# Optimization experiments

Hardware: AMD Instinct MI355X
Metric: run time of the kernel (lower is better)

Reference implementation:

```python
import jax, jax.numpy as jnp
import numpy as np

B, L, D, H, R = 2, 128, 256, 8, 4
DK = D // H  # 32
EPS = 1e-6


def setup_inputs() -> dict:
    key = jax.random.key(0)
    ks = jax.random.split(key, 12)
    q = jax.random.normal(ks[0], (B, L, D), jnp.float32)
    k = jax.random.normal(ks[1], (B, L, D), jnp.float32)
    v = jax.random.normal(ks[2], (B, L, D), jnp.float32)
    t = jnp.sort(jax.random.uniform(ks[3], (B, L), jnp.float32), axis=-1)
    omega = jax.random.uniform(ks[4], (B, L, L), jnp.float32)
    mask = jnp.triu(jnp.ones((L, L), bool), 1)  # True = masked (causal)
    xav = (2.0 / (D + D)) ** 0.5
    Wq = jax.random.normal(ks[5], (D, H * DK), jnp.float32) * xav
    Wk = jax.random.normal(ks[6], (D, H * DK), jnp.float32) * xav
    Wv = jax.random.normal(ks[7], (D, H * DK), jnp.float32) * xav
    s = jax.random.uniform(ks[8], (R,), jnp.float32) + 0.1  # ODE time-decay scales
    fc_w = jax.random.normal(ks[9], (H * DK, D), jnp.float32) * xav
    fc_b = jnp.zeros((D,), jnp.float32)
    ln_g = jnp.ones((D,), jnp.float32)
    ln_b = jnp.zeros((D,), jnp.float32)
    return {"q": q, "k": k, "v": v, "t": t, "omega": omega, "mask": mask,
            "Wq": Wq, "Wk": Wk, "Wv": Wv, "s": s,
            "fc_w": fc_w, "fc_b": fc_b, "ln_g": ln_g, "ln_b": ln_b}


def _ode_proj(x, W, phi):
    # x: (B,L,D), W: (D,H*DK), phi: (B,L,L,R) time kernel
    p = x @ W                                       # (B,L,H*DK)
    y = p[:, None, :, None, :] * phi[..., None]     # (B,L,L,R,H*DK)
    y = y.reshape(B, L, L, R, H, DK)
    return y.transpose(0, 4, 1, 2, 3, 5)            # (B,H,L,L,R,DK)


def reference(q, k, v, t, omega, mask, Wq, Wk, Wv, s, fc_w, fc_b, ln_g, ln_b):
    temp = DK ** 0.5
    residual = q
    # pre-LayerNorm on q (normalize_before=True)
    mu = q.mean(-1, keepdims=True)
    var = q.var(-1, keepdims=True)
    qn = (q - mu) / jnp.sqrt(var + EPS) * ln_g + ln_b
    # continuous-time kernel phi[b,i,j,r] = exp(-|t_i - t_j| * s_r)
    dt = jnp.abs(t[:, :, None] - t[:, None, :])     # (B,L,L)
    phi = jnp.exp(-dt[..., None] * s)               # (B,L,L,R)
    q6 = _ode_proj(qn, Wq, phi)                     # (B,H,L,L,R,DK)
    k6 = _ode_proj(k, Wk, phi)
    v6 = _ode_proj(v, Wv, phi)
    # attn = (q/temp * k * omega).sum(-1).sum(-1)
    attn = jnp.einsum('bhijrd,bhijrd,bij->bhij', q6 / temp, k6, omega)
    attn = jnp.where(mask[None, None, :, :], -1e9, attn)
    attn = jax.nn.softmax(attn, axis=-1)            # (B,H,L,L)
    vsum = v6.sum(axis=4)                           # sum over R -> (B,H,L,L,DK)
    out = jnp.einsum('bhij,bhijd->bhid', attn, vsum)  # (B,H,L,DK)
    out = out.transpose(0, 2, 1, 3).reshape(B, L, H * DK)
    out = out @ fc_w + fc_b + residual              # dropout = identity (eval)
    return (out, attn)
```

## Files before the change

kernel.cpp:

```cpp
#include <hip/hip_runtime.h>

#define B_  2
#define L_  128
#define D_  256
#define H_  8
#define R_  4
#define DK_ 32
#define BL_ (B_*L_)
#define SXP 260

__device__ __forceinline__ float wredsum64(float v) {
    #pragma unroll
    for (int m = 32; m >= 1; m >>= 1) v += __shfl_xor(v, m, 64);
    return v;
}
__device__ __forceinline__ float wredmax64(float v) {
    #pragma unroll
    for (int m = 32; m >= 1; m >>= 1) v = fmaxf(v, __shfl_xor(v, m, 64));
    return v;
}

__global__ __launch_bounds__(256) void k_proj(
    const float* __restrict__ q, const float* __restrict__ k, const float* __restrict__ v,
    const float* __restrict__ Wq, const float* __restrict__ Wk, const float* __restrict__ Wv,
    const float* __restrict__ ln_g, const float* __restrict__ ln_b,
    float* __restrict__ pv, float* __restrict__ qkpart)
{
    const int blk = blockIdx.x;
    const int rowTile = blk >> 4;
    const int cg = blk & 15;
    const int rbase = rowTile * 4;
    const int tid = threadIdx.x;

    __shared__ __align__(16) float sx[3][4 * SXP];
    __shared__ __align__(16) float partF[16 * 4 * 16];
    __shared__ float spq[4][16], spk[4][16];

    {
        const int r = tid >> 6, f4c = tid & 63;
        #pragma unroll
        for (int p = 0; p < 3; ++p) {
            const float* src = (p == 0 ? q : (p == 1 ? k : v)) + (size_t)(rbase + r) * D_;
            *reinterpret_cast<float4*>(&sx[p][r * SXP + f4c * 4]) =
                reinterpret_cast<const float4*>(src)[f4c];
        }
    }
    __syncthreads();

    {
        const int r = tid >> 6, lane = tid & 63;
        float x0 = sx[0][r * SXP + lane];
        float x1 = sx[0][r * SXP + lane + 64];
        float x2 = sx[0][r * SXP + lane + 128];
        float x3 = sx[0][r * SXP + lane + 192];
        float s1 = x0 + x1 + x2 + x3;
        float s2 = x0*x0 + x1*x1 + x2*x2 + x3*x3;
        #pragma unroll
        for (int m = 32; m >= 1; m >>= 1) {
            s1 += __shfl_xor(s1, m, 64);
            s2 += __shfl_xor(s2, m, 64);
        }
        const float mu = s1 * (1.0f / D_);
        const float rs = rsqrtf(s2 * (1.0f / D_) - mu * mu + 1e-6f);
        sx[0][r * SXP + lane      ] = (x0 - mu) * rs * ln_g[lane      ] + ln_b[lane      ];
        sx[0][r * SXP + lane +  64] = (x1 - mu) * rs * ln_g[lane +  64] + ln_b[lane +  64];
        sx[0][r * SXP + lane + 128] = (x2 - mu) * rs * ln_g[lane + 128] + ln_b[lane + 128];
        sx[0][r * SXP + lane + 192] = (x3 - mu) * rs * ln_g[lane + 192] + ln_b[lane + 192];
    }
    __syncthreads();

    const int kg  = tid >> 4;
    const int row = (tid >> 2) & 3;
    const int c4  = tid & 3;
    const int gc4 = cg * 4 + c4;
    const int kbase = kg * 16;

    #pragma unroll
    for (int m = 0; m < 3; ++m) {
        const float4* W4 = reinterpret_cast<const float4*>(m == 0 ? Wq : (m == 1 ? Wk : Wv));
        float4 a = {0, 0, 0, 0};
        #pragma unroll
        for (int kk = 0; kk < 16; ++kk) {
            const int kr = kbase + kk;
            const float x = sx[m][row * SXP + kr];
            const float4 w = W4[kr * 64 + gc4];
            a.x += x * w.x; a.y += x * w.y; a.z += x * w.z; a.w += x * w.w;
        }
        *reinterpret_cast<float4*>(&partF[(kg * 16 + row * 4 + c4) * 4]) = a;
        __syncthreads();
        if (tid < 64) {
            const int rr = tid >> 4, cc = tid & 15;
            float sum = 0.f;
            #pragma unroll
            for (int g = 0; g < 16; ++g) sum += partF[g * 64 + rr * 16 + cc];
            if      (m == 0) spq[rr][cc] = sum;
            else if (m == 1) spk[rr][cc] = sum;
            else             pv[(size_t)(rbase + rr) * D_ + cg * 16 + cc] = sum;
        }
        __syncthreads();
    }

    if (tid < 64) {
        const int rr = tid >> 4, cc = tid & 15;
        float d = spq[rr][cc] * spk[rr][cc];
        #pragma unroll
        for (int m = 8; m >= 1; m >>= 1) d += __shfl_xor(d, m, 64);
        if (cc == 0) qkpart[(size_t)(rbase + rr) * 16 + cg] = d;
    }
}

__global__ __launch_bounds__(256) void k_attn(
    const float* __restrict__ t, const float* __restrict__ omega, const float* __restrict__ s,
    const float* __restrict__ pv, const float* __restrict__ qkpart,
    float* __restrict__ mid, float* __restrict__ dout)
{
    const int blk = blockIdx.x;
    const int b     = blk >> 8;
    const int itile = (blk >> 3) & 31;
    const int h     = blk & 7;
    const int ibase = itile * 4;
    const int tid = threadIdx.x;

    __shared__ __align__(16) float sQKp[L_ * 16];
    __shared__ __align__(16) float sQKh[L_];
    __shared__ __align__(16) float sOm[4 * L_];
    __shared__ __align__(16) float sPhi[4 * L_], sPsi[4 * L_];
    __shared__ __align__(16) float sAttn[4 * L_];
    __shared__ __align__(16) float partF[32 * 4 * 32];
    __shared__ float st[L_], sS[R_];

    {
        const float4* qkp4 = reinterpret_cast<const float4*>(qkpart + (size_t)b * L_ * 16);
        reinterpret_cast<float4*>(sQKp)[tid]       = qkp4[tid];
        reinterpret_cast<float4*>(sQKp)[tid + 256] = qkp4[tid + 256];
        if (tid < 128)
            reinterpret_cast<float4*>(sOm)[tid] =
                reinterpret_cast<const float4*>(omega + ((size_t)(b * L_ + ibase)) * L_)[tid];
        if (tid < 32)
            reinterpret_cast<float4*>(st)[tid] =
                reinterpret_cast<const float4*>(t + (size_t)b * L_)[tid];
        if (tid < R_) sS[tid] = s[tid];
    }
    __syncthreads();

    if (tid < 128) sQKh[tid] = sQKp[tid * 16 + 2 * h] + sQKp[tid * 16 + 2 * h + 1];
    #pragma unroll
    for (int p = 0; p < 2; ++p) {
        const int idx = tid + p * 256;
        const int w = idx >> 7, j = idx & 127;
        const float dtv = fabsf(st[ibase + w] - st[j]);
        float Phi = 0.f, Psi = 0.f;
        #pragma unroll
        for (int r = 0; r < R_; ++r) {
            const float e = expf(-dtv * sS[r]);
            Phi += e;
            Psi += e * e;
        }
        sPhi[idx] = Phi;
        sPsi[idx] = Psi;
    }
    __syncthreads();

    const int w = tid >> 6, lane = tid & 63;
    const int i = ibase + w;
    {
        const float invtemp = 0.17677669529663687f;
        const int j0 = lane, j1 = lane + 64;
        float l0 = (j0 <= i) ? sOm[w*L_ + j0] * sPsi[w*L_ + j0] * sQKh[j0] * invtemp : -3.0e38f;
        float l1 = (j1 <= i) ? sOm[w*L_ + j1] * sPsi[w*L_ + j1] * sQKh[j1] * invtemp : -3.0e38f;
        const float mx = wredmax64(fmaxf(l0, l1));
        const float e0 = (j0 <= i) ? expf(l0 - mx) : 0.f;
        const float e1 = (j1 <= i) ? expf(l1 - mx) : 0.f;
        const float inv = 1.0f / wredsum64(e0 + e1);
        const float a0 = e0 * inv, a1 = e1 * inv;
        sAttn[w*L_ + j0] = a0;
        sAttn[w*L_ + j1] = a1;
        const size_t ab = (size_t)BL_ * D_ + (((size_t)(b * H_ + h) * L_ + i) * L_);
        dout[ab + j0] = a0;
        dout[ab + j1] = a1;
    }
    __syncthreads();

    {
        const int jg = tid >> 3, c4 = tid & 7;
        const int gc4 = h * 8 + c4;
        const float4* pv4 = reinterpret_cast<const float4*>(pv + (size_t)b * L_ * D_);
        float4 acc[4];
        #pragma unroll
        for (int ww = 0; ww < 4; ++ww) acc[ww] = make_float4(0, 0, 0, 0);
        #pragma unroll
        for (int jj = 0; jj < 4; ++jj) {
            const int j = jg + jj * 32;
            const float4 p = pv4[j * 64 + gc4];
            #pragma unroll
            for (int ww = 0; ww < 4; ++ww) {
                const float wgt = sAttn[ww*L_ + j] * sPhi[ww*L_ + j];
                acc[ww].x += wgt * p.x; acc[ww].y += wgt * p.y;
                acc[ww].z += wgt * p.z; acc[ww].w += wgt * p.w;
            }
        }
        #pragma unroll
        for (int ww = 0; ww < 4; ++ww)
            *reinterpret_cast<float4*>(&partF[(jg * 32 + ww * 8 + c4) * 4]) = acc[ww];
    }
    __syncthreads();
    if (tid < 128) {
        const int ww = tid >> 5, cc = tid & 31;
        float sum = 0.f;
        #pragma unroll
        for (int g = 0; g < 32; ++g) sum += partF[g * 128 + ww * 32 + cc];
        mid[((size_t)(b * L_ + ibase + ww)) * D_ + h * 32 + cc] = sum;
    }
}

__global__ __launch_bounds__(256) void k_fc(
    const float* __restrict__ q, const float* __restrict__ fc_w, const float* __restrict__ fc_b,
    const float* __restrict__ mid, float* __restrict__ dout)
{
    const int blk = blockIdx.x;
    const int rowTile = blk >> 4;
    const int cg = blk & 15;
    const int rbase = rowTile * 4;
    const int tid = threadIdx.x;

    __shared__ __align__(16) float smid[4 * SXP];
    __shared__ __align__(16) float partF[16 * 4 * 16];

    {
        const int r = tid >> 6, f4c = tid & 63;
        *reinterpret_cast<float4*>(&smid[r * SXP + f4c * 4]) =
            reinterpret_cast<const float4*>(mid + (size_t)(rbase + r) * D_)[f4c];
    }
    __syncthreads();

    const int kg  = tid >> 4;
    const int row = (tid >> 2) & 3;
    const int c4  = tid & 3;
    const int gc4 = cg * 4 + c4;
    const int kbase = kg * 16;
    const float4* fw4 = reinterpret_cast<const float4*>(fc_w);
    float4 a = {0, 0, 0, 0};
    #pragma unroll
    for (int kk = 0; kk < 16; ++kk) {
        const int kr = kbase + kk;
        const float x = smid[row * SXP + kr];
        const float4 wv = fw4[kr * 64 + gc4];
        a.x += x * wv.x; a.y += x * wv.y; a.z += x * wv.z; a.w += x * wv.w;
    }
    *reinterpret_cast<float4*>(&partF[(kg * 16 + row * 4 + c4) * 4]) = a;
    __syncthreads();

    if (tid < 64) {
        const int rr = tid >> 4, cc = tid & 15;
        const int col = cg * 16 + cc;
        float sum = fc_b[col] + q[(size_t)(rbase + rr) * D_ + col];
        #pragma unroll
        for (int g = 0; g < 16; ++g) sum += partF[g * 64 + rr * 16 + cc];
        dout[(size_t)(rbase + rr) * D_ + col] = sum;
    }
}

extern "C" void kernel_launch(void* const* d_in, const int* in_sizes, int n_in,
                              void* d_out, int out_size, void* d_ws, size_t ws_size,
                              hipStream_t stream) {
    const float* q     = (const float*)d_in[0];
    const float* k     = (const float*)d_in[1];
    const float* v     = (const float*)d_in[2];
    const float* t     = (const float*)d_in[3];
    const float* omega = (const float*)d_in[4];
    const float* Wq    = (const float*)d_in[6];
    const float* Wk    = (const float*)d_in[7];
    const float* Wv    = (const float*)d_in[8];
    const float* s     = (const float*)d_in[9];
    const float* fc_w  = (const float*)d_in[10];
    const float* fc_b  = (const float*)d_in[11];
    const float* ln_g  = (const float*)d_in[12];
    const float* ln_b  = (const float*)d_in[13];

    float* ws     = (float*)d_ws;
    float* pv     = ws;
    float* qkpart = ws + 65536;
    float* mid    = ws + 69632;
    float* out    = (float*)d_out;

    hipLaunchKernelGGL(k_proj, dim3(1024), dim3(256), 0, stream,
                       q, k, v, Wq, Wk, Wv, ln_g, ln_b, pv, qkpart);
    hipLaunchKernelGGL(k_attn, dim3(512), dim3(256), 0, stream,
                       t, omega, s, pv, qkpart, mid, out);
    hipLaunchKernelGGL(k_fc, dim3(1024), dim3(256), 0, stream,
                       q, fc_w, fc_b, mid, out);
}
```

Measured before the change: 96.96 us.

## Fuse output projection into attention kernel via per-head atomic accumulation

Removes the separate fc kernel. The projection kernel now initializes the output with residual plus bias. The attention kernel keeps its per-head 4x32 result in shared memory, multiplies it by the matching 32-row slice of fc_w, and atomically adds the partial into the output. This saves one kernel launch and the round trip of the intermediate buffer through memory. In exchange it adds 8-way atomic contention per output element and makes the float summation order nondeterministic.

```diff
diff --git a/kernel.cpp b/kernel.cpp
--- a/kernel.cpp
+++ b/kernel.cpp
@@ -24,7 +24,8 @@
     const float* __restrict__ q, const float* __restrict__ k, const float* __restrict__ v,
     const float* __restrict__ Wq, const float* __restrict__ Wk, const float* __restrict__ Wv,
     const float* __restrict__ ln_g, const float* __restrict__ ln_b,
-    float* __restrict__ pv, float* __restrict__ qkpart)
+    const float* __restrict__ fc_b,
+    float* __restrict__ pv, float* __restrict__ qkpart, float* __restrict__ dout)
 {
     const int blk = blockIdx.x;
     const int rowTile = blk >> 4;
@@ -44,6 +45,13 @@
             *reinterpret_cast<float4*>(&sx[p][r * SXP + f4c * 4]) =
                 reinterpret_cast<const float4*>(src)[f4c];
         }
+    }
+
+    if (tid < 64) {
+        const int rr = tid >> 4, cc = tid & 15;
+        const int col = cg * 16 + cc;
+        const size_t off = (size_t)(rbase + rr) * D_ + col;
+        dout[off] = q[off] + fc_b[col];
     }
     __syncthreads();
 
@@ -112,7 +120,7 @@
 __global__ __launch_bounds__(256) void k_attn(
     const float* __restrict__ t, const float* __restrict__ omega, const float* __restrict__ s,
     const float* __restrict__ pv, const float* __restrict__ qkpart,
-    float* __restrict__ mid, float* __restrict__ dout)
+    const float* __restrict__ fc_w, float* __restrict__ dout)
 {
     const int blk = blockIdx.x;
     const int b     = blk >> 8;
@@ -128,6 +136,7 @@
     __shared__ __align__(16) float sAttn[4 * L_];
     __shared__ __align__(16) float partF[32 * 4 * 32];
     __shared__ float st[L_], sS[R_];
+    __shared__ float sMid[4][32];
 
     {
         const float4* qkp4 = reinterpret_cast<const float4*>(qkpart + (size_t)b * L_ * 16);
@@ -147,8 +156,8 @@
     #pragma unroll
     for (int p = 0; p < 2; ++p) {
         const int idx = tid + p * 256;
-        const int w = idx >> 7, j = idx & 127;
-        const float dtv = fabsf(st[ibase + w] - st[j]);
+        const int wi = idx >> 7, j = idx & 127;
+        const float dtv = fabsf(st[ibase + wi] - st[j]);
         float Phi = 0.f, Psi = 0.f;
         #pragma unroll
         for (int r = 0; r < R_; ++r) {
@@ -209,54 +218,24 @@
         float sum = 0.f;
         #pragma unroll
         for (int g = 0; g < 32; ++g) sum += partF[g * 128 + ww * 32 + cc];
-        mid[((size_t)(b * L_ + ibase + ww)) * D_ + h * 32 + cc] = sum;
-    }
-}
-
-__global__ __launch_bounds__(256) void k_fc(
-    const float* __restrict__ q, const float* __restrict__ fc_w, const float* __restrict__ fc_b,
-    const float* __restrict__ mid, float* __restrict__ dout)
-{
-    const int blk = blockIdx.x;
-    const int rowTile = blk >> 4;
-    const int cg = blk & 15;
-    const int rbase = rowTile * 4;
-    const int tid = threadIdx.x;
-
-    __shared__ __align__(16) float smid[4 * SXP];
-    __shared__ __align__(16) float partF[16 * 4 * 16];
-
-    {
-        const int r = tid >> 6, f4c = tid & 63;
-        *reinterpret_cast<float4*>(&smid[r * SXP + f4c * 4]) =
-            reinterpret_cast<const float4*>(mid + (size_t)(rbase + r) * D_)[f4c];
-    }
-    __syncthreads();
-
-    const int kg  = tid >> 4;
-    const int row = (tid >> 2) & 3;
-    const int c4  = tid & 3;
-    const int gc4 = cg * 4 + c4;
-    const int kbase = kg * 16;
-    const float4* fw4 = reinterpret_cast<const float4*>(fc_w);
-    float4 a = {0, 0, 0, 0};
-    #pragma unroll
-    for (int kk = 0; kk < 16; ++kk) {
-        const int kr = kbase + kk;
-        const float x = smid[row * SXP + kr];
-        const float4 wv = fw4[kr * 64 + gc4];
-        a.x += x * wv.x; a.y += x * wv.y; a.z += x * wv.z; a.w += x * wv.w;
-    }
-    *reinterpret_cast<float4*>(&partF[(kg * 16 + row * 4 + c4) * 4]) = a;
-    __syncthreads();
-
-    if (tid < 64) {
-        const int rr = tid >> 4, cc = tid & 15;
-        const int col = cg * 16 + cc;
-        float sum = fc_b[col] + q[(size_t)(rbase + rr) * D_ + col];
-        #pragma unroll
-        for (int g = 0; g < 16; ++g) sum += partF[g * 64 + rr * 16 + cc];
-        dout[(size_t)(rbase + rr) * D_ + col] = sum;
+        sMid[ww][cc] = sum;
+    }
+    __syncthreads();
+
+    {
+        const float4* fw4 = reinterpret_cast<const float4*>(fc_w);
+        float4 a = {0, 0, 0, 0};
+        #pragma unroll
+        for (int cc = 0; cc < 32; ++cc) {
+            const float x = sMid[w][cc];
+            const float4 wv = fw4[(h * 32 + cc) * 64 + lane];
+            a.x += x * wv.x; a.y += x * wv.y; a.z += x * wv.z; a.w += x * wv.w;
+        }
+        float* op = dout + (size_t)(b * L_ + i) * D_ + lane * 4;
+        atomicAdd(op + 0, a.x);
+        atomicAdd(op + 1, a.y);
+        atomicAdd(op + 2, a.z);
+        atomicAdd(op + 3, a.w);
     }
 }
 
@@ -280,13 +259,10 @@
     float* ws     = (float*)d_ws;
     float* pv     = ws;
     float* qkpart = ws + 65536;
-    float* mid    = ws + 69632;
     float* out    = (float*)d_out;
 
     hipLaunchKernelGGL(k_proj, dim3(1024), dim3(256), 0, stream,
-                       q, k, v, Wq, Wk, Wv, ln_g, ln_b, pv, qkpart);
+                       q, k, v, Wq, Wk, Wv, ln_g, ln_b, fc_b, pv, qkpart, out);
     hipLaunchKernelGGL(k_attn, dim3(512), dim3(256), 0, stream,
-                       t, omega, s, pv, qkpart, mid, out);
-    hipLaunchKernelGGL(k_fc, dim3(1024), dim3(256), 0, stream,
-                       q, fc_w, fc_b, mid, out);
-}
+                       t, omega, s, pv, qkpart, fc_w, out);
+}
```

Measured after the change: 100.6 us. 3.7% more time.
